# Kernel optimization log

Measured on AMD Instinct MI355X. Metric: run time of the kernel, lower is better.

## Reference

```python
import jax, jax.numpy as jnp
import numpy as np

NUM_GRAPHS = 128


def _gcn_conv(x, W, b, src, dst, norm, n_nodes):
    # PyG GCNConv: linear transform, then symmetric-normalized scatter-add aggregation
    h = x @ W                                  # [N, out]
    msg = norm[:, None] * h[src]               # [E+N, out] gathered messages
    out = jax.ops.segment_sum(msg, dst, num_segments=n_nodes)
    return out + b


def setup_inputs() -> dict:
    key = jax.random.key(0)
    ks = jax.random.split(key, 12)
    N, E, H, GE, C = 100000, 1000000, 64, 64, 5
    x = jax.random.normal(ks[0], (N, 2), dtype=jnp.float32)
    edge_index = jax.random.randint(ks[1], (2, E), 0, N, dtype=jnp.int32)
    batch = jnp.sort(jax.random.randint(ks[2], (N,), 0, NUM_GRAPHS, dtype=jnp.int32))
    graph_embedding = jax.random.normal(ks[3], (NUM_GRAPHS, GE), dtype=jnp.float32)
    s = lambda k, shape, fan: jax.random.normal(k, shape, dtype=jnp.float32) * (1.0 / np.sqrt(fan))
    W1 = s(ks[4], (2, H), 2); b1 = jnp.zeros((H,), jnp.float32)
    W2 = s(ks[5], (H, H), H); b2 = jnp.zeros((H,), jnp.float32)
    W3 = s(ks[6], (H, H), H); b3 = jnp.zeros((H,), jnp.float32)
    Wl = s(ks[7], (H + GE, C), H + GE); bl = jnp.zeros((C,), jnp.float32)
    return {"x": x, "edge_index": edge_index, "batch": batch,
            "graph_embedding": graph_embedding,
            "W1": W1, "b1": b1, "W2": W2, "b2": b2, "W3": W3, "b3": b3,
            "Wl": Wl, "bl": bl}


def reference(x, edge_index, batch, graph_embedding, W1, b1, W2, b2, W3, b3, Wl, bl):
    N = x.shape[0]
    loops = jnp.arange(N, dtype=edge_index.dtype)
    src = jnp.concatenate([edge_index[0], loops])   # add self-loops
    dst = jnp.concatenate([edge_index[1], loops])
    deg = jax.ops.segment_sum(jnp.ones_like(dst, dtype=x.dtype), dst, num_segments=N)
    dinv = jnp.where(deg > 0, jax.lax.rsqrt(deg), 0.0)
    norm = dinv[src] * dinv[dst]                    # [E+N]

    h = jax.nn.relu(_gcn_conv(x, W1, b1, src, dst, norm, N))
    h = jax.nn.relu(_gcn_conv(h, W2, b2, src, dst, norm, N))
    h = _gcn_conv(h, W3, b3, src, dst, norm, N)

    # global mean pool over graphs
    sums = jax.ops.segment_sum(h, batch, num_segments=NUM_GRAPHS)
    cnts = jax.ops.segment_sum(jnp.ones((N,), x.dtype), batch, num_segments=NUM_GRAPHS)
    pooled = sums / jnp.maximum(cnts, 1.0)[:, None]

    z = jnp.concatenate([pooled, graph_embedding], axis=1) @ Wl + bl
    return jax.nn.log_softmax(z, axis=1)
```

## Files before the change

### kernel.cpp

```cpp
#include <hip/hip_runtime.h>
#include <hip/hip_bf16.h>
#include <math.h>

#define NG 128
#define CHUNKB 4096
#define NBIN 512
#define EWIN 256
#define STAGE_CAP 6144

typedef __attribute__((ext_vector_type(8))) short short8;
typedef __attribute__((ext_vector_type(4))) float float4v;
typedef __attribute__((ext_vector_type(4))) uint uint4v;

__global__ void k_bin_hist(const int* __restrict__ dst, int* __restrict__ hist,
                           int e, int nb, float* __restrict__ sums,
                           const float* __restrict__ W2, const float* __restrict__ W3,
                           __hip_bfloat16* __restrict__ Wf2, __hip_bfloat16* __restrict__ Wf3) {
    __shared__ int h[NBIN];
    int blk = blockIdx.x;
    if (blk >= nb) {
        int ex = blk - nb;
        if (ex == 0) {
            for (int i = threadIdx.x; i < NG * 64; i += 256) sums[i] = 0.0f;
        } else {
            const float* W = (ex == 2) ? W3 : W2;
            __hip_bfloat16* Wf = (ex == 2) ? Wf3 : Wf2;
            for (int t = threadIdx.x; t < 512; t += 256) {
                int c = t >> 6, l = t & 63;
                int jt = c >> 1, half = c & 1, nn = l & 15, q = l >> 4;
                #pragma unroll
                for (int j = 0; j < 8; j++) {
                    int k = half * 32 + q * 8 + j;
                    Wf[t * 8 + j] = __float2bfloat16(W[k * 64 + jt * 16 + nn]);
                }
            }
        }
        return;
    }
    for (int i = threadIdx.x; i < NBIN; i += 256) h[i] = 0;
    __syncthreads();
    int base = blk * CHUNKB;
    int lim = e - base; if (lim > CHUNKB) lim = CHUNKB;
    for (int k = threadIdx.x; k < lim; k += 256)
        atomicAdd(&h[dst[base + k] >> 8], 1);
    __syncthreads();
    for (int b = threadIdx.x; b < NBIN; b += 256) hist[b * nb + blk] = h[b];
}

__global__ void __launch_bounds__(512) genscan1(int* __restrict__ a, int* __restrict__ bsums, int n) {
    __shared__ int s[512];
    int tid = threadIdx.x;
    int i = blockIdx.x * 512 + tid;
    int v = (i < n) ? a[i] : 0;
    s[tid] = v;
    __syncthreads();
    for (int d = 1; d < 512; d <<= 1) {
        int t = (tid >= d) ? s[tid - d] : 0;
        __syncthreads();
        s[tid] += t;
        __syncthreads();
    }
    if (i < n) a[i] = s[tid] - v;
    if (tid == 511) bsums[blockIdx.x] = s[511];
}

__global__ void __launch_bounds__(512) genscan2(int* __restrict__ bsums, int nb) {
    __shared__ int s[512];
    int tid = threadIdx.x;
    int v = (tid < nb) ? bsums[tid] : 0;
    s[tid] = v;
    __syncthreads();
    for (int d = 1; d < 512; d <<= 1) {
        int t = (tid >= d) ? s[tid - d] : 0;
        __syncthreads();
        s[tid] += t;
        __syncthreads();
    }
    if (tid < nb) bsums[tid] = s[tid] - v;
}

__global__ void k_bin_scatter(const int* __restrict__ srcs, const int* __restrict__ dsts,
                              const int* __restrict__ offsets, const int* __restrict__ bsums,
                              int2* __restrict__ outbuf, int e, int nb) {
    __shared__ int hcnt[NBIN];
    __shared__ int lstart[NBIN];
    __shared__ int ss[256];
    __shared__ int2 stage[CHUNKB];
    int tid = threadIdx.x, blk = blockIdx.x, base = blk * CHUNKB;
    int lim = e - base; if (lim > CHUNKB) lim = CHUNKB;
    for (int i = tid; i < NBIN; i += 256) hcnt[i] = 0;
    __syncthreads();
    for (int k = tid; k < lim; k += 256)
        atomicAdd(&hcnt[dsts[base + k] >> 8], 1);
    __syncthreads();
    int c0 = hcnt[2 * tid], c1 = hcnt[2 * tid + 1];
    int sum = c0 + c1;
    ss[tid] = sum;
    __syncthreads();
    for (int d = 1; d < 256; d <<= 1) {
        int t = (tid >= d) ? ss[tid - d] : 0;
        __syncthreads();
        ss[tid] += t;
        __syncthreads();
    }
    int excl = ss[tid] - sum;
    lstart[2 * tid] = excl;
    lstart[2 * tid + 1] = excl + c0;
    __syncthreads();
    hcnt[2 * tid] = excl;
    hcnt[2 * tid + 1] = excl + c0;
    __syncthreads();
    for (int k = tid; k < lim; k += 256) {
        int2 ed = make_int2(srcs[base + k], dsts[base + k]);
        int p = atomicAdd(&hcnt[ed.y >> 8], 1);
        stage[p] = ed;
    }
    __syncthreads();
    for (int i = tid; i < NBIN; i += 256) {
        int gi = i * nb + blk;
        lstart[i] = offsets[gi] + bsums[gi >> 9] - lstart[i];
    }
    __syncthreads();
    for (int p = tid; p < lim; p += 256) {
        int2 ed = stage[p];
        outbuf[lstart[ed.y >> 8] + p] = ed;
    }
}

__global__ void k_csrAB(const int2* __restrict__ ebuck, const int* __restrict__ offsets,
                        const int* __restrict__ bsums, const float* __restrict__ x,
                        int* __restrict__ row_ptr, float* __restrict__ dinv,
                        float2* __restrict__ xs, int* __restrict__ csr,
                        int n, int nb, int e_total) {
    __shared__ int lcnt[256];
    __shared__ int ssc[256];
    __shared__ int rstart[256];
    __shared__ int2 stage[STAGE_CAP];
    int b = blockIdx.x, tid = threadIdx.x, n0 = b << 8;
    lcnt[tid] = 0;
    __syncthreads();
    int i0 = b * nb, i1 = (b + 1) * nb;
    int e0 = offsets[i0] + bsums[i0 >> 9];
    int e1 = offsets[i1] + bsums[i1 >> 9];
    int cnt = e1 - e0;
    bool fast = (cnt <= STAGE_CAP);
    if (fast) {
        for (int i = e0 + tid; i < e1; i += 256) {
            int2 ed = ebuck[i];
            stage[i - e0] = ed;
            atomicAdd(&lcnt[ed.y - n0], 1);
        }
    } else {
        for (int i = e0 + tid; i < e1; i += 256)
            atomicAdd(&lcnt[ebuck[i].y - n0], 1);
    }
    __syncthreads();
    int v = lcnt[tid];
    ssc[tid] = v;
    __syncthreads();
    for (int d = 1; d < 256; d <<= 1) {
        int t = (tid >= d) ? ssc[tid - d] : 0;
        __syncthreads();
        ssc[tid] += t;
        __syncthreads();
    }
    int rs = e0 + ssc[tid] - v;
    rstart[tid] = rs;
    int node = n0 + tid;
    if (node < n) {
        row_ptr[node] = rs;
        float dv = rsqrtf((float)v + 1.0f);
        dinv[node] = dv;
        const float2* x2 = (const float2*)x;
        float2 xi = x2[node];
        xs[node] = make_float2(xi.x * dv, xi.y * dv);
        if (node == n - 1) row_ptr[n] = e_total;
    }
    lcnt[tid] = 0;
    __syncthreads();
    if (fast) {
        for (int i = tid; i < cnt; i += 256) {
            int2 ed = stage[i];
            int li = ed.y - n0;
            int r = atomicAdd(&lcnt[li], 1);
            csr[rstart[li] + r] = ed.x;
        }
    } else {
        for (int i = e0 + tid; i < e1; i += 256) {
            int2 ed = ebuck[i];
            int li = ed.y - n0;
            int r = atomicAdd(&lcnt[li], 1);
            csr[rstart[li] + r] = ed.x;
        }
    }
}

__global__ void k_layer1(const int* __restrict__ row_ptr, const int* __restrict__ edges,
                         const float2* __restrict__ xs, const float* __restrict__ dinv,
                         const float* __restrict__ W1, const float* __restrict__ b1,
                         __hip_bfloat16* __restrict__ h, int n) {
    __shared__ float w1s[128];
    __shared__ float b1s[64];
    if (threadIdx.x < 128) w1s[threadIdx.x] = W1[threadIdx.x];
    if (threadIdx.x < 64) b1s[threadIdx.x] = b1[threadIdx.x];
    __syncthreads();
    int i = blockIdx.x * blockDim.x + threadIdx.x;
    if (i >= n) return;
    float dd = dinv[i];
    float2 xi = xs[i];
    float a0 = xi.x, a1 = xi.y;
    int lo = row_ptr[i], hi = row_ptr[i + 1];
    int k = lo;
    for (; k + 4 <= hi; k += 4) {
        int s0 = edges[k], s1 = edges[k + 1], s2 = edges[k + 2], s3 = edges[k + 3];
        float2 v0 = xs[s0], v1 = xs[s1], v2 = xs[s2], v3 = xs[s3];
        a0 += v0.x + v1.x + v2.x + v3.x;
        a1 += v0.y + v1.y + v2.y + v3.y;
    }
    for (; k < hi; k++) {
        float2 v = xs[edges[k]];
        a0 += v.x;
        a1 += v.y;
    }
    a0 *= dd; a1 *= dd;
    short8* hv = reinterpret_cast<short8*>(h + (size_t)i * 64);
    #pragma unroll
    for (int g = 0; g < 8; g++) {
        short8 pack;
        #pragma unroll
        for (int j = 0; j < 8; j++) {
            int col = g * 8 + j;
            float v = fmaxf(a0 * w1s[col] + a1 * w1s[64 + col] + b1s[col], 0.0f);
            v *= dd;
            __hip_bfloat16 bv = __float2bfloat16(v);
            pack[j] = *reinterpret_cast<short*>(&bv);
        }
        hv[g] = pack;
    }
}

static __device__ __forceinline__ void acc8(float* a, uint4v v) {
    #pragma unroll
    for (int i = 0; i < 4; i++) {
        uint u = v[i];
        a[2 * i]     += __int_as_float(u << 16);
        a[2 * i + 1] += __int_as_float(u & 0xffff0000u);
    }
}

template <bool FAST>
static __device__ __forceinline__ void agg_group(int lo, int cnt, int mc, int c,
        const int* __restrict__ gE, const int* EW, int wave_lo,
        const uint4v* __restrict__ hin4, float* acc) {
    for (int j = 0; j < mc; j += 2) {
        bool ok0 = j < cnt, ok1 = j + 1 < cnt;
        int e0 = ok0 ? lo + j : wave_lo;
        int e1 = ok1 ? lo + j + 1 : wave_lo;
        int s0 = FAST ? EW[e0 - wave_lo] : gE[e0];
        int s1 = FAST ? EW[e1 - wave_lo] : gE[e1];
        uint4v v0 = hin4[(size_t)s0 * 8 + c];
        uint4v v1 = hin4[(size_t)s1 * 8 + c];
        if (!ok0) v0 = (uint4v){0u, 0u, 0u, 0u};
        if (!ok1) v1 = (uint4v){0u, 0u, 0u, 0u};
        acc8(acc, v0);
        acc8(acc, v1);
    }
}

template <int RELU, int POOL>
__global__ void __launch_bounds__(64, 8) k_aggLin(const int* __restrict__ row_ptr,
                                                  const int* __restrict__ edges,
                                                  const __hip_bfloat16* __restrict__ hin,
                                                  const float* __restrict__ dinv,
                                                  const __hip_bfloat16* __restrict__ Wf,
                                                  const float* __restrict__ b,
                                                  __hip_bfloat16* __restrict__ hout,
                                                  const int* __restrict__ batch,
                                                  float* __restrict__ sums, int n) {
    __shared__ __attribute__((aligned(16))) __hip_bfloat16 T[16 * 72];
    __shared__ int EW[EWIN];
    int lane = threadIdx.x;
    int nb0 = blockIdx.x * 16;
    if (nb0 >= n) return;
    int g = lane >> 3;
    int c = lane & 7;
    const uint4v* hin4 = reinterpret_cast<const uint4v*>(hin);

    int bidx = nb0 + (lane < 16 ? lane : 16);
    if (bidx > n) bidx = n;
    int rp = row_ptr[bidx];
    int wave_lo = __shfl(rp, 0);
    int wave_hi = __shfl(rp, 16);
    int cnt_all = wave_hi - wave_lo;
    bool fast = (cnt_all <= EWIN);
    if (fast)
        for (int i = lane; i < cnt_all; i += 64) EW[i] = edges[wave_lo + i];

    #pragma unroll
    for (int h8 = 0; h8 < 2; h8++) {
        int nn = h8 * 8 + g;
        int node = nb0 + nn;
        float acc[8] = {0.f, 0.f, 0.f, 0.f, 0.f, 0.f, 0.f, 0.f};
        int lo = __shfl(rp, nn);
        int hi = __shfl(rp, nn + 1);
        int cnt = (node < n) ? (hi - lo) : 0;
        int mc = cnt;
        mc = max(mc, __shfl_xor(mc, 8));
        mc = max(mc, __shfl_xor(mc, 16));
        mc = max(mc, __shfl_xor(mc, 32));
        if (node < n)
            acc8(acc, hin4[(size_t)node * 8 + c]);
        if (fast) agg_group<true >(lo, cnt, mc, c, edges, EW, wave_lo, hin4, acc);
        else      agg_group<false>(lo, cnt, mc, c, edges, EW, wave_lo, hin4, acc);
        float dv = (node < n) ? dinv[node] : 0.0f;
        uint4v pk;
        #pragma unroll
        for (int i = 0; i < 4; i++) {
            __hip_bfloat16 bx = __float2bfloat16(acc[2 * i] * dv);
            __hip_bfloat16 by = __float2bfloat16(acc[2 * i + 1] * dv);
            pk[i] = (uint)(*reinterpret_cast<unsigned short*>(&bx)) |
                    ((uint)(*reinterpret_cast<unsigned short*>(&by)) << 16);
        }
        *reinterpret_cast<uint4v*>(&T[nn * 72 + c * 8]) = pk;
    }

    int m = lane & 15, q = lane >> 4;
    short8 a0 = *reinterpret_cast<const short8*>(&T[m * 72 + q * 8]);
    short8 a1 = *reinterpret_cast<const short8*>(&T[m * 72 + 32 + q * 8]);
    int lastn = nb0 + 15 < n ? nb0 + 15 : n - 1;
    bool onegraph = POOL && (nb0 + 15 < n) && (batch[nb0] == batch[lastn]);
    int gA = POOL ? batch[nb0] : 0;
    float dvs[4];
    if (!POOL) {
        #pragma unroll
        for (int r = 0; r < 4; r++) {
            int node = nb0 + q * 4 + r;
            dvs[r] = node < n ? dinv[node] : 0.0f;
        }
    }
    #pragma unroll
    for (int jt = 0; jt < 4; jt++) {
        short8 bf0 = *reinterpret_cast<const short8*>(Wf + ((size_t)(jt * 2 + 0) * 64 + lane) * 8);
        short8 bf1 = *reinterpret_cast<const short8*>(Wf + ((size_t)(jt * 2 + 1) * 64 + lane) * 8);
        float4v d = {0.0f, 0.0f, 0.0f, 0.0f};
        d = __builtin_amdgcn_mfma_f32_16x16x32_bf16(a0, bf0, d, 0, 0, 0);
        d = __builtin_amdgcn_mfma_f32_16x16x32_bf16(a1, bf1, d, 0, 0, 0);
        float bias = b[jt * 16 + m];
        if (POOL) {
            if (onegraph) {
                float s = (d[0] + bias) + (d[1] + bias) + (d[2] + bias) + (d[3] + bias);
                s += __shfl_xor(s, 16);
                s += __shfl_xor(s, 32);
                if (q == 0) atomicAdd(&sums[gA * 64 + jt * 16 + m], s);
            } else {
                #pragma unroll
                for (int r = 0; r < 4; r++) {
                    int node = nb0 + q * 4 + r;
                    if (node < n)
                        atomicAdd(&sums[batch[node] * 64 + jt * 16 + m], d[r] + bias);
                }
            }
        } else {
            #pragma unroll
            for (int r = 0; r < 4; r++) {
                int node = nb0 + q * 4 + r;
                if (node < n) {
                    float v = d[r] + bias;
                    if (RELU) v = fmaxf(v, 0.0f);
                    v *= dvs[r];
                    hout[(size_t)node * 64 + jt * 16 + m] = __float2bfloat16(v);
                }
            }
        }
    }
}

__device__ inline int lower_bound_i(const int* __restrict__ a, int n, int key) {
    int lo = 0, hi = n;
    while (lo < hi) {
        int mid = (lo + hi) >> 1;
        if (a[mid] < key) lo = mid + 1; else hi = mid;
    }
    return lo;
}

__global__ void k_head(const float* __restrict__ sums, const int* __restrict__ batch,
                       const float* __restrict__ ge, const float* __restrict__ Wl,
                       const float* __restrict__ bl, float* __restrict__ out,
                       int n, int ng) {
    int g = blockIdx.x * blockDim.x + threadIdx.x;
    if (g < ng) {
        int lo = lower_bound_i(batch, n, g);
        int hi = lower_bound_i(batch, n, g + 1);
        float c = fmaxf((float)(hi - lo), 1.0f);
        float z[5];
        for (int cl = 0; cl < 5; cl++) z[cl] = bl[cl];
        for (int k = 0; k < 64; k++) {
            float p = sums[g * 64 + k] / c;
            for (int cl = 0; cl < 5; cl++) z[cl] += p * Wl[k * 5 + cl];
        }
        for (int k = 0; k < 64; k++) {
            float p = ge[g * 64 + k];
            for (int cl = 0; cl < 5; cl++) z[cl] += p * Wl[(64 + k) * 5 + cl];
        }
        float m = z[0];
        for (int cl = 1; cl < 5; cl++) m = fmaxf(m, z[cl]);
        float s = 0.0f;
        for (int cl = 0; cl < 5; cl++) s += expf(z[cl] - m);
        float lse = m + logf(s);
        for (int cl = 0; cl < 5; cl++) out[g * 5 + cl] = z[cl] - lse;
    }
}

#define ALIGN16(x) (((x) + 15) & ~(size_t)15)

extern "C" void kernel_launch(void* const* d_in, const int* in_sizes, int n_in,
                              void* d_out, int out_size, void* d_ws, size_t ws_size,
                              hipStream_t stream) {
    const float* x    = (const float*)d_in[0];
    const int*   ei   = (const int*)d_in[1];
    const int*   batch= (const int*)d_in[2];
    const float* ge   = (const float*)d_in[3];
    const float* W1   = (const float*)d_in[4];
    const float* b1   = (const float*)d_in[5];
    const float* W2   = (const float*)d_in[6];
    const float* b2   = (const float*)d_in[7];
    const float* W3   = (const float*)d_in[8];
    const float* b3   = (const float*)d_in[9];
    const float* Wl   = (const float*)d_in[10];
    const float* bl   = (const float*)d_in[11];
    float* out = (float*)d_out;

    const int N = in_sizes[0] / 2;
    const int E = in_sizes[1] / 2;
    const int* src = ei;
    const int* dst = ei + E;
    const int NBUK = (N + 255) >> 8;
    const int nbC  = (E + CHUNKB - 1) / CHUNKB;

    char* wsb = (char*)d_ws;
    float* dinv   = (float*)wsb;                wsb += ALIGN16((size_t)N * 4);
    float2* xs    = (float2*)wsb;               wsb += ALIGN16((size_t)N * 8);
    __hip_bfloat16* h16 = (__hip_bfloat16*)wsb;  wsb += ALIGN16((size_t)64 * N * 2);
    __hip_bfloat16* buf2= (__hip_bfloat16*)wsb;  wsb += ALIGN16((size_t)64 * N * 2);
    float* sums   = (float*)wsb;                wsb += ALIGN16((size_t)NG * 64 * 4);
    __hip_bfloat16* Wf2 = (__hip_bfloat16*)wsb; wsb += ALIGN16((size_t)4096 * 2);
    __hip_bfloat16* Wf3 = (__hip_bfloat16*)wsb; wsb += ALIGN16((size_t)4096 * 2);
    int2*  ebuck  = (int2*)wsb;                 wsb += ALIGN16((size_t)E * 8);
    int*   csr    = (int*)wsb;                  wsb += ALIGN16((size_t)E * 4);
    int*   row_ptr= (int*)wsb;                  wsb += ALIGN16((size_t)(N + 1) * 4);
    int*   hist   = (int*)wsb;                  wsb += ALIGN16((size_t)NBIN * nbC * 4);
    int*   bsums  = (int*)wsb;                  wsb += 512 * 4;

    const int BS = 256;
    int gN   = (N + BS - 1) / BS;
    int gF   = (N + 15) / 16;
    int nH   = NBIN * nbC;
    int gH   = (nH + 511) / 512;

    k_bin_hist<<<nbC + 3, BS, 0, stream>>>(dst, hist, E, nbC, sums, W2, W3, Wf2, Wf3);
    genscan1<<<gH, 512, 0, stream>>>(hist, bsums, nH);
    genscan2<<<1, 512, 0, stream>>>(bsums, gH);
    k_bin_scatter<<<nbC, BS, 0, stream>>>(src, dst, hist, bsums, ebuck, E, nbC);
    k_csrAB<<<NBUK, BS, 0, stream>>>(ebuck, hist, bsums, x, row_ptr, dinv, xs, csr,
                                     N, nbC, E);

    k_layer1<<<gN, BS, 0, stream>>>(row_ptr, csr, xs, dinv, W1, b1, h16, N);

    k_aggLin<1, 0><<<gF, 64, 0, stream>>>(row_ptr, csr, h16, dinv, Wf2, b2, buf2,
                                          nullptr, nullptr, N);

    k_aggLin<0, 1><<<gF, 64, 0, stream>>>(row_ptr, csr, buf2, dinv, Wf3, b3, nullptr,
                                          batch, sums, N);

    k_head<<<1, 128, 0, stream>>>(sums, batch, ge, Wl, bl, out, N, NG);
}
```

Before: 199.7 us.

## Pack bucketed edges to 32 bits, halve scatter chunk, fuse head via ticket

Bucketed edges are now stored as one packed int (low 8 bits of dst in the top byte, src in the low 24 bits) instead of an int2. This halves the traffic of the scatter and CSR-build passes. The binning chunk size is halved, giving more scatter blocks and less shared memory per block. The final classifier head is folded into the last aggregation kernel: a last-block-done ticket lets the final block compute the log-softmax, removing one launch. The packing assumes node ids fit in 24 bits.

After: 320.2 us. 1.6x slower.

```diff
diff --git a/kernel.cpp b/kernel.cpp
--- a/kernel.cpp
+++ b/kernel.cpp
@@ -3,7 +3,7 @@
 #include <math.h>
 
 #define NG 128
-#define CHUNKB 4096
+#define CHUNKB 2048
 #define NBIN 512
 #define EWIN 256
 #define STAGE_CAP 6144
@@ -15,13 +15,15 @@
 __global__ void k_bin_hist(const int* __restrict__ dst, int* __restrict__ hist,
                            int e, int nb, float* __restrict__ sums,
                            const float* __restrict__ W2, const float* __restrict__ W3,
-                           __hip_bfloat16* __restrict__ Wf2, __hip_bfloat16* __restrict__ Wf3) {
+                           __hip_bfloat16* __restrict__ Wf2, __hip_bfloat16* __restrict__ Wf3,
+                           int* __restrict__ ticket) {
     __shared__ int h[NBIN];
     int blk = blockIdx.x;
     if (blk >= nb) {
         int ex = blk - nb;
         if (ex == 0) {
             for (int i = threadIdx.x; i < NG * 64; i += 256) sums[i] = 0.0f;
+            if (threadIdx.x == 0) *ticket = 0;
         } else {
             const float* W = (ex == 2) ? W3 : W2;
             __hip_bfloat16* Wf = (ex == 2) ? Wf3 : Wf2;
@@ -81,11 +83,12 @@
 
 __global__ void k_bin_scatter(const int* __restrict__ srcs, const int* __restrict__ dsts,
                               const int* __restrict__ offsets, const int* __restrict__ bsums,
-                              int2* __restrict__ outbuf, int e, int nb) {
+                              int* __restrict__ outbuf, int e, int nb) {
     __shared__ int hcnt[NBIN];
     __shared__ int lstart[NBIN];
     __shared__ int ss[256];
-    __shared__ int2 stage[CHUNKB];
+    __shared__ int stage[CHUNKB];
+    __shared__ int sbuck[CHUNKB];
     int tid = threadIdx.x, blk = blockIdx.x, base = blk * CHUNKB;
     int lim = e - base; if (lim > CHUNKB) lim = CHUNKB;
     for (int i = tid; i < NBIN; i += 256) hcnt[i] = 0;
@@ -111,9 +114,11 @@
     hcnt[2 * tid + 1] = excl + c0;
     __syncthreads();
     for (int k = tid; k < lim; k += 256) {
-        int2 ed = make_int2(srcs[base + k], dsts[base + k]);
-        int p = atomicAdd(&hcnt[ed.y >> 8], 1);
-        stage[p] = ed;
+        int s = srcs[base + k], d = dsts[base + k];
+        int bk = d >> 8;
+        int p = atomicAdd(&hcnt[bk], 1);
+        stage[p] = ((d & 255) << 24) | s;
+        sbuck[p] = bk;
     }
     __syncthreads();
     for (int i = tid; i < NBIN; i += 256) {
@@ -121,13 +126,11 @@
         lstart[i] = offsets[gi] + bsums[gi >> 9] - lstart[i];
     }
     __syncthreads();
-    for (int p = tid; p < lim; p += 256) {
-        int2 ed = stage[p];
-        outbuf[lstart[ed.y >> 8] + p] = ed;
-    }
-}
-
-__global__ void k_csrAB(const int2* __restrict__ ebuck, const int* __restrict__ offsets,
+    for (int p = tid; p < lim; p += 256)
+        outbuf[lstart[sbuck[p]] + p] = stage[p];
+}
+
+__global__ void k_csrAB(const int* __restrict__ ebuck, const int* __restrict__ offsets,
                         const int* __restrict__ bsums, const float* __restrict__ x,
                         int* __restrict__ row_ptr, float* __restrict__ dinv,
                         float2* __restrict__ xs, int* __restrict__ csr,
@@ -135,7 +138,7 @@
     __shared__ int lcnt[256];
     __shared__ int ssc[256];
     __shared__ int rstart[256];
-    __shared__ int2 stage[STAGE_CAP];
+    __shared__ int stage[STAGE_CAP];
     int b = blockIdx.x, tid = threadIdx.x, n0 = b << 8;
     lcnt[tid] = 0;
     __syncthreads();
@@ -146,13 +149,13 @@
     bool fast = (cnt <= STAGE_CAP);
     if (fast) {
         for (int i = e0 + tid; i < e1; i += 256) {
-            int2 ed = ebuck[i];
-            stage[i - e0] = ed;
-            atomicAdd(&lcnt[ed.y - n0], 1);
+            int p = ebuck[i];
+            stage[i - e0] = p;
+            atomicAdd(&lcnt[(uint)p >> 24], 1);
         }
     } else {
         for (int i = e0 + tid; i < e1; i += 256)
-            atomicAdd(&lcnt[ebuck[i].y - n0], 1);
+            atomicAdd(&lcnt[(uint)ebuck[i] >> 24], 1);
     }
     __syncthreads();
     int v = lcnt[tid];
@@ -180,17 +183,17 @@
     __syncthreads();
     if (fast) {
         for (int i = tid; i < cnt; i += 256) {
-            int2 ed = stage[i];
-            int li = ed.y - n0;
+            int p = stage[i];
+            int li = (uint)p >> 24;
             int r = atomicAdd(&lcnt[li], 1);
-            csr[rstart[li] + r] = ed.x;
+            csr[rstart[li] + r] = p & 0xFFFFFF;
         }
     } else {
         for (int i = e0 + tid; i < e1; i += 256) {
-            int2 ed = ebuck[i];
-            int li = ed.y - n0;
+            int p = ebuck[i];
+            int li = (uint)p >> 24;
             int r = atomicAdd(&lcnt[li], 1);
-            csr[rstart[li] + r] = ed.x;
+            csr[rstart[li] + r] = p & 0xFFFFFF;
         }
     }
 }
@@ -268,147 +271,147 @@
 }
 
 template <int RELU, int POOL>
-__global__ void __launch_bounds__(64, 8) k_aggLin(const int* __restrict__ row_ptr,
-                                                  const int* __restrict__ edges,
-                                                  const __hip_bfloat16* __restrict__ hin,
-                                                  const float* __restrict__ dinv,
-                                                  const __hip_bfloat16* __restrict__ Wf,
-                                                  const float* __restrict__ b,
-                                                  __hip_bfloat16* __restrict__ hout,
-                                                  const int* __restrict__ batch,
-                                                  float* __restrict__ sums, int n) {
+__global__ void __launch_bounds__(64, 8) k_aggLin(
+        const int* __restrict__ row_ptr, const int* __restrict__ edges,
+        const __hip_bfloat16* __restrict__ hin, const float* __restrict__ dinv,
+        const __hip_bfloat16* __restrict__ Wf, const float* __restrict__ b,
+        __hip_bfloat16* __restrict__ hout, const int* __restrict__ batch,
+        float* __restrict__ sums, int n,
+        const float* __restrict__ ge, const float* __restrict__ Wl,
+        const float* __restrict__ bl, float* __restrict__ out,
+        int* __restrict__ ticket) {
     __shared__ __attribute__((aligned(16))) __hip_bfloat16 T[16 * 72];
     __shared__ int EW[EWIN];
+    __shared__ int lastflag;
     int lane = threadIdx.x;
     int nb0 = blockIdx.x * 16;
-    if (nb0 >= n) return;
-    int g = lane >> 3;
-    int c = lane & 7;
-    const uint4v* hin4 = reinterpret_cast<const uint4v*>(hin);
-
-    int bidx = nb0 + (lane < 16 ? lane : 16);
-    if (bidx > n) bidx = n;
-    int rp = row_ptr[bidx];
-    int wave_lo = __shfl(rp, 0);
-    int wave_hi = __shfl(rp, 16);
-    int cnt_all = wave_hi - wave_lo;
-    bool fast = (cnt_all <= EWIN);
-    if (fast)
-        for (int i = lane; i < cnt_all; i += 64) EW[i] = edges[wave_lo + i];
-
-    #pragma unroll
-    for (int h8 = 0; h8 < 2; h8++) {
-        int nn = h8 * 8 + g;
-        int node = nb0 + nn;
-        float acc[8] = {0.f, 0.f, 0.f, 0.f, 0.f, 0.f, 0.f, 0.f};
-        int lo = __shfl(rp, nn);
-        int hi = __shfl(rp, nn + 1);
-        int cnt = (node < n) ? (hi - lo) : 0;
-        int mc = cnt;
-        mc = max(mc, __shfl_xor(mc, 8));
-        mc = max(mc, __shfl_xor(mc, 16));
-        mc = max(mc, __shfl_xor(mc, 32));
-        if (node < n)
-            acc8(acc, hin4[(size_t)node * 8 + c]);
-        if (fast) agg_group<true >(lo, cnt, mc, c, edges, EW, wave_lo, hin4, acc);
-        else      agg_group<false>(lo, cnt, mc, c, edges, EW, wave_lo, hin4, acc);
-        float dv = (node < n) ? dinv[node] : 0.0f;
-        uint4v pk;
+    if (nb0 < n) {
+        int g = lane >> 3;
+        int c = lane & 7;
+        const uint4v* hin4 = reinterpret_cast<const uint4v*>(hin);
+
+        int bidx = nb0 + (lane < 16 ? lane : 16);
+        if (bidx > n) bidx = n;
+        int rp = row_ptr[bidx];
+        int wave_lo = __shfl(rp, 0);
+        int wave_hi = __shfl(rp, 16);
+        int cnt_all = wave_hi - wave_lo;
+        bool fast = (cnt_all <= EWIN);
+        if (fast)
+            for (int i = lane; i < cnt_all; i += 64) EW[i] = edges[wave_lo + i];
+
         #pragma unroll
-        for (int i = 0; i < 4; i++) {
-            __hip_bfloat16 bx = __float2bfloat16(acc[2 * i] * dv);
-            __hip_bfloat16 by = __float2bfloat16(acc[2 * i + 1] * dv);
-            pk[i] = (uint)(*reinterpret_cast<unsigned short*>(&bx)) |
-                    ((uint)(*reinterpret_cast<unsigned short*>(&by)) << 16);
-        }
-        *reinterpret_cast<uint4v*>(&T[nn * 72 + c * 8]) = pk;
-    }
-
-    int m = lane & 15, q = lane >> 4;
-    short8 a0 = *reinterpret_cast<const short8*>(&T[m * 72 + q * 8]);
-    short8 a1 = *reinterpret_cast<const short8*>(&T[m * 72 + 32 + q * 8]);
-    int lastn = nb0 + 15 < n ? nb0 + 15 : n - 1;
-    bool onegraph = POOL && (nb0 + 15 < n) && (batch[nb0] == batch[lastn]);
-    int gA = POOL ? batch[nb0] : 0;
-    float dvs[4];
-    if (!POOL) {
+        for (int h8 = 0; h8 < 2; h8++) {
+            int nn = h8 * 8 + g;
+            int node = nb0 + nn;
+            float acc[8] = {0.f, 0.f, 0.f, 0.f, 0.f, 0.f, 0.f, 0.f};
+            int lo = __shfl(rp, nn);
+            int hi = __shfl(rp, nn + 1);
+            int cnt = (node < n) ? (hi - lo) : 0;
+            int mc = cnt;
+            mc = max(mc, __shfl_xor(mc, 8));
+            mc = max(mc, __shfl_xor(mc, 16));
+            mc = max(mc, __shfl_xor(mc, 32));
+            if (node < n)
+                acc8(acc, hin4[(size_t)node * 8 + c]);
+            if (fast) agg_group<true >(lo, cnt, mc, c, edges, EW, wave_lo, hin4, acc);
+            else      agg_group<false>(lo, cnt, mc, c, edges, EW, wave_lo, hin4, acc);
+            float dv = (node < n) ? dinv[node] : 0.0f;
+            uint4v pk;
+            #pragma unroll
+            for (int i = 0; i < 4; i++) {
+                __hip_bfloat16 bx = __float2bfloat16(acc[2 * i] * dv);
+                __hip_bfloat16 by = __float2bfloat16(acc[2 * i + 1] * dv);
+                pk[i] = (uint)(*reinterpret_cast<unsigned short*>(&bx)) |
+                        ((uint)(*reinterpret_cast<unsigned short*>(&by)) << 16);
+            }
+            *reinterpret_cast<uint4v*>(&T[nn * 72 + c * 8]) = pk;
+        }
+
+        int m = lane & 15, q = lane >> 4;
+        short8 a0 = *reinterpret_cast<const short8*>(&T[m * 72 + q * 8]);
+        short8 a1 = *reinterpret_cast<const short8*>(&T[m * 72 + 32 + q * 8]);
+        int lastn = nb0 + 15 < n ? nb0 + 15 : n - 1;
+        bool onegraph = POOL && (nb0 + 15 < n) && (batch[nb0] == batch[lastn]);
+        int gA = POOL ? batch[nb0] : 0;
+        float dvs[4];
+        if (!POOL) {
+            #pragma unroll
+            for (int r = 0; r < 4; r++) {
+                int node = nb0 + q * 4 + r;
+                dvs[r] = node < n ? dinv[node] : 0.0f;
+            }
+        }
         #pragma unroll
-        for (int r = 0; r < 4; r++) {
-            int node = nb0 + q * 4 + r;
-            dvs[r] = node < n ? dinv[node] : 0.0f;
-        }
-    }
-    #pragma unroll
-    for (int jt = 0; jt < 4; jt++) {
-        short8 bf0 = *reinterpret_cast<const short8*>(Wf + ((size_t)(jt * 2 + 0) * 64 + lane) * 8);
-        short8 bf1 = *reinterpret_cast<const short8*>(Wf + ((size_t)(jt * 2 + 1) * 64 + lane) * 8);
-        float4v d = {0.0f, 0.0f, 0.0f, 0.0f};
-        d = __builtin_amdgcn_mfma_f32_16x16x32_bf16(a0, bf0, d, 0, 0, 0);
-        d = __builtin_amdgcn_mfma_f32_16x16x32_bf16(a1, bf1, d, 0, 0, 0);
-        float bias = b[jt * 16 + m];
-        if (POOL) {
-            if (onegraph) {
-                float s = (d[0] + bias) + (d[1] + bias) + (d[2] + bias) + (d[3] + bias);
-                s += __shfl_xor(s, 16);
-                s += __shfl_xor(s, 32);
-                if (q == 0) atomicAdd(&sums[gA * 64 + jt * 16 + m], s);
+        for (int jt = 0; jt < 4; jt++) {
+            short8 bf0 = *reinterpret_cast<const short8*>(Wf + ((size_t)(jt * 2 + 0) * 64 + lane) * 8);
+            short8 bf1 = *reinterpret_cast<const short8*>(Wf + ((size_t)(jt * 2 + 1) * 64 + lane) * 8);
+            float4v d = {0.0f, 0.0f, 0.0f, 0.0f};
+            d = __builtin_amdgcn_mfma_f32_16x16x32_bf16(a0, bf0, d, 0, 0, 0);
+            d = __builtin_amdgcn_mfma_f32_16x16x32_bf16(a1, bf1, d, 0, 0, 0);
+            float bias = b[jt * 16 + m];
+            if (POOL) {
+                if (onegraph) {
+                    float s = (d[0] + bias) + (d[1] + bias) + (d[2] + bias) + (d[3] + bias);
+                    s += __shfl_xor(s, 16);
+                    s += __shfl_xor(s, 32);
+                    if (q == 0) atomicAdd(&sums[gA * 64 + jt * 16 + m], s);
+                } else {
+                    #pragma unroll
+                    for (int r = 0; r < 4; r++) {
+                        int node = nb0 + q * 4 + r;
+                        if (node < n)
+                            atomicAdd(&sums[batch[node] * 64 + jt * 16 + m], d[r] + bias);
+                    }
+                }
             } else {
                 #pragma unroll
                 for (int r = 0; r < 4; r++) {
                     int node = nb0 + q * 4 + r;
-                    if (node < n)
-                        atomicAdd(&sums[batch[node] * 64 + jt * 16 + m], d[r] + bias);
+                    if (node < n) {
+                        float v = d[r] + bias;
+                        if (RELU) v = fmaxf(v, 0.0f);
+                        v *= dvs[r];
+                        hout[(size_t)node * 64 + jt * 16 + m] = __float2bfloat16(v);
+                    }
                 }
             }
-        } else {
-            #pragma unroll
-            for (int r = 0; r < 4; r++) {
-                int node = nb0 + q * 4 + r;
-                if (node < n) {
-                    float v = d[r] + bias;
-                    if (RELU) v = fmaxf(v, 0.0f);
-                    v *= dvs[r];
-                    hout[(size_t)node * 64 + jt * 16 + m] = __float2bfloat16(v);
+        }
+    }
+    if (POOL) {
+        __threadfence();
+        if (threadIdx.x == 0) {
+            int t = atomicAdd(ticket, 1);
+            lastflag = (t == (int)gridDim.x - 1);
+        }
+        __syncthreads();
+        if (lastflag) {
+            __threadfence();
+            for (int gq = threadIdx.x; gq < NG; gq += 64) {
+                int lo = 0, hi = n;
+                while (lo < hi) { int mid = (lo + hi) >> 1; if (batch[mid] < gq) lo = mid + 1; else hi = mid; }
+                int l0 = lo; lo = 0; hi = n;
+                while (lo < hi) { int mid = (lo + hi) >> 1; if (batch[mid] < gq + 1) lo = mid + 1; else hi = mid; }
+                float cdenom = fmaxf((float)(lo - l0), 1.0f);
+                float z[5];
+                for (int cl = 0; cl < 5; cl++) z[cl] = bl[cl];
+                for (int k = 0; k < 64; k++) {
+                    float p = __hip_atomic_load(&sums[gq * 64 + k], __ATOMIC_RELAXED,
+                                                __HIP_MEMORY_SCOPE_AGENT) / cdenom;
+                    for (int cl = 0; cl < 5; cl++) z[cl] += p * Wl[k * 5 + cl];
                 }
+                for (int k = 0; k < 64; k++) {
+                    float p = ge[gq * 64 + k];
+                    for (int cl = 0; cl < 5; cl++) z[cl] += p * Wl[(64 + k) * 5 + cl];
+                }
+                float mm = z[0];
+                for (int cl = 1; cl < 5; cl++) mm = fmaxf(mm, z[cl]);
+                float s = 0.0f;
+                for (int cl = 0; cl < 5; cl++) s += expf(z[cl] - mm);
+                float lse = mm + logf(s);
+                for (int cl = 0; cl < 5; cl++) out[gq * 5 + cl] = z[cl] - lse;
             }
         }
-    }
-}
-
-__device__ inline int lower_bound_i(const int* __restrict__ a, int n, int key) {
-    int lo = 0, hi = n;
-    while (lo < hi) {
-        int mid = (lo + hi) >> 1;
-        if (a[mid] < key) lo = mid + 1; else hi = mid;
-    }
-    return lo;
-}
-
-__global__ void k_head(const float* __restrict__ sums, const int* __restrict__ batch,
-                       const float* __restrict__ ge, const float* __restrict__ Wl,
-                       const float* __restrict__ bl, float* __restrict__ out,
-                       int n, int ng) {
-    int g = blockIdx.x * blockDim.x + threadIdx.x;
-    if (g < ng) {
-        int lo = lower_bound_i(batch, n, g);
-        int hi = lower_bound_i(batch, n, g + 1);
-        float c = fmaxf((float)(hi - lo), 1.0f);
-        float z[5];
-        for (int cl = 0; cl < 5; cl++) z[cl] = bl[cl];
-        for (int k = 0; k < 64; k++) {
-            float p = sums[g * 64 + k] / c;
-            for (int cl = 0; cl < 5; cl++) z[cl] += p * Wl[k * 5 + cl];
-        }
-        for (int k = 0; k < 64; k++) {
-            float p = ge[g * 64 + k];
-            for (int cl = 0; cl < 5; cl++) z[cl] += p * Wl[(64 + k) * 5 + cl];
-        }
-        float m = z[0];
-        for (int cl = 1; cl < 5; cl++) m = fmaxf(m, z[cl]);
-        float s = 0.0f;
-        for (int cl = 0; cl < 5; cl++) s += expf(z[cl] - m);
-        float lse = m + logf(s);
-        for (int cl = 0; cl < 5; cl++) out[g * 5 + cl] = z[cl] - lse;
     }
 }
 
@@ -446,11 +449,12 @@
     float* sums   = (float*)wsb;                wsb += ALIGN16((size_t)NG * 64 * 4);
     __hip_bfloat16* Wf2 = (__hip_bfloat16*)wsb; wsb += ALIGN16((size_t)4096 * 2);
     __hip_bfloat16* Wf3 = (__hip_bfloat16*)wsb; wsb += ALIGN16((size_t)4096 * 2);
-    int2*  ebuck  = (int2*)wsb;                 wsb += ALIGN16((size_t)E * 8);
+    int*   ebuck  = (int*)wsb;                  wsb += ALIGN16((size_t)E * 4);
     int*   csr    = (int*)wsb;                  wsb += ALIGN16((size_t)E * 4);
     int*   row_ptr= (int*)wsb;                  wsb += ALIGN16((size_t)(N + 1) * 4);
     int*   hist   = (int*)wsb;                  wsb += ALIGN16((size_t)NBIN * nbC * 4);
     int*   bsums  = (int*)wsb;                  wsb += 512 * 4;
+    int*   ticket = (int*)wsb;                  wsb += 16;
 
     const int BS = 256;
     int gN   = (N + BS - 1) / BS;
@@ -458,7 +462,8 @@
     int nH   = NBIN * nbC;
     int gH   = (nH + 511) / 512;
 
-    k_bin_hist<<<nbC + 3, BS, 0, stream>>>(dst, hist, E, nbC, sums, W2, W3, Wf2, Wf3);
+    k_bin_hist<<<nbC + 3, BS, 0, stream>>>(dst, hist, E, nbC, sums, W2, W3, Wf2, Wf3,
+                                           ticket);
     genscan1<<<gH, 512, 0, stream>>>(hist, bsums, nH);
     genscan2<<<1, 512, 0, stream>>>(bsums, gH);
     k_bin_scatter<<<nbC, BS, 0, stream>>>(src, dst, hist, bsums, ebuck, E, nbC);
@@ -468,10 +473,10 @@
     k_layer1<<<gN, BS, 0, stream>>>(row_ptr, csr, xs, dinv, W1, b1, h16, N);
 
     k_aggLin<1, 0><<<gF, 64, 0, stream>>>(row_ptr, csr, h16, dinv, Wf2, b2, buf2,
-                                          nullptr, nullptr, N);
+                                          nullptr, nullptr, N,
+                                          nullptr, nullptr, nullptr, nullptr, nullptr);
 
     k_aggLin<0, 1><<<gF, 64, 0, stream>>>(row_ptr, csr, buf2, dinv, Wf3, b3, nullptr,
-                                          batch, sums, N);
-
-    k_head<<<1, 128, 0, stream>>>(sums, batch, ge, Wl, bl, out, N, NG);
-}
+                                          batch, sums, N,
+                                          ge, Wl, bl, out, ticket);
+}
```
